# Kernel tuning notes

Hardware: AMD Instinct MI355X
Metric: run time of the kernel (lower is better)

The kernel has to match this reference:

```python
import jax, jax.numpy as jnp
import numpy as np

N, F, T, H, E, OUT, HEADS = 20000, 32, 12, 64, 320000, 12, 2


def setup_inputs() -> dict:
    key = jax.random.key(0)
    ks = iter(jax.random.split(key, 40))

    def nrm(shape, scale):
        return jax.random.normal(next(ks), shape, jnp.float32) * scale

    g0 = 2 * H + F   # gate input dim, cell 0
    g1 = 2 * H + H   # gate input dim, cell 1
    inp = {
        "x": nrm((N, F, T), 1.0),
        "edge_index": jax.random.randint(next(ks), (2, E), 0, N, dtype=jnp.int32),
        "edge_attr": jax.random.uniform(next(ks), (E, 2), dtype=jnp.float32),
        # cell 0: GCNConv + GRU gates (weights stored [in, out])
        "Wg0": nrm((F, H), F ** -0.5), "bg0": nrm((H,), 0.02),
        "Wu0": nrm((g0, H), g0 ** -0.5), "bu0": nrm((H,), 0.02),
        "Wr0": nrm((g0, H), g0 ** -0.5), "br0": nrm((H,), 0.02),
        "Wc0": nrm((g0, H), g0 ** -0.5), "bc0": nrm((H,), 0.02),
        # cell 1
        "Wg1": nrm((H, H), H ** -0.5), "bg1": nrm((H,), 0.02),
        "Wu1": nrm((g1, H), g1 ** -0.5), "bu1": nrm((H,), 0.02),
        "Wr1": nrm((g1, H), g1 ** -0.5), "br1": nrm((H,), 0.02),
        "Wc1": nrm((g1, H), g1 ** -0.5), "bc1": nrm((H,), 0.02),
        # temporal multi-head attention (torch layout: [out, in])
        "in_proj_w": nrm((3 * H, H), H ** -0.5), "in_proj_b": nrm((3 * H,), 0.02),
        "out_proj_w": nrm((H, H), H ** -0.5), "out_proj_b": nrm((H,), 0.02),
        # output head ([in, out])
        "out_w": nrm((H, OUT), H ** -0.5), "out_b": nrm((OUT,), 0.02),
    }
    return inp


def reference(x, edge_index, edge_attr,
              Wg0, bg0, Wu0, bu0, Wr0, br0, Wc0, bc0,
              Wg1, bg1, Wu1, bu1, Wr1, br1, Wc1, bc1,
              in_proj_w, in_proj_b, out_proj_w, out_proj_b,
              out_w, out_b):
    n, f, t = x.shape
    h_dim = Wg0.shape[1]
    src, dst = edge_index[0], edge_index[1]
    w = edge_attr[:, -1]

    # GCN normalization with self-loops (PyG gcn_norm)
    loop = jnp.arange(n)
    src_all = jnp.concatenate([src, loop])
    dst_all = jnp.concatenate([dst, loop])
    w_all = jnp.concatenate([w, jnp.ones((n,), x.dtype)])
    deg = jax.ops.segment_sum(w_all, dst_all, num_segments=n)
    dinv = jnp.where(deg > 0, jax.lax.rsqrt(deg), 0.0)
    norm = dinv[src_all] * w_all * dinv[dst_all]  # [E+N]

    def gcn(xi, W, b):
        xw = xi @ W  # [N, H]
        msg = norm[:, None] * xw[src_all]  # gather from sources
        return jax.ops.segment_sum(msg, dst_all, num_segments=n) + b

    def cell(xi, h, W, b, Wu, bu, Wr, br, Wc, bc):
        g = jax.nn.sigmoid(gcn(xi, W, b))
        zu = jnp.concatenate([xi, g, h], axis=-1)
        u = jax.nn.sigmoid(zu @ Wu + bu)
        r = jax.nn.sigmoid(zu @ Wr + br)
        zc = jnp.concatenate([xi, g, r * h], axis=-1)
        c = jnp.tanh(zc @ Wc + bc)
        return u * h + (1.0 - u) * c

    def step(carry, x_t):
        h0, h1 = carry
        h0 = cell(x_t, h0, Wg0, bg0, Wu0, bu0, Wr0, br0, Wc0, bc0)
        h1 = cell(h0, h1, Wg1, bg1, Wu1, bu1, Wr1, br1, Wc1, bc1)
        return (h0, h1), h1

    x_seq = jnp.transpose(x, (2, 0, 1))  # [T, N, F]
    h0 = jnp.zeros((n, h_dim), x.dtype)
    _, h_seq = jax.lax.scan(step, (h0, h0), x_seq)  # [T, N, H] (== [S, B, H])

    # temporal multi-head self-attention per node
    heads = HEADS
    dh = h_dim // heads
    qkv = h_seq @ in_proj_w.T + in_proj_b  # [T, N, 3H]
    q, k, v = jnp.split(qkv, 3, axis=-1)

    def split_heads(a):
        return jnp.transpose(a.reshape(t, n, heads, dh), (1, 2, 0, 3))  # [N, h, T, dh]

    q, k, v = split_heads(q), split_heads(k), split_heads(v)
    scores = jnp.einsum('nhtd,nhsd->nhts', q, k) / jnp.sqrt(jnp.asarray(dh, x.dtype))
    attn = jax.nn.softmax(scores, axis=-1)
    o = jnp.einsum('nhts,nhsd->nhtd', attn, v)
    o = jnp.transpose(o, (2, 0, 1, 3)).reshape(t, n, h_dim)
    o = o @ out_proj_w.T + out_proj_b  # [T, N, H]

    h_attn = o.mean(axis=0)  # agg='mean' over sequence -> [N, H]
    return h_attn @ out_w + out_b  # [N, OUT]
```

## Files before the change

kernel.cpp:

```cpp
#include <hip/hip_runtime.h>
#include <math.h>

#define NN 20000
#define FF 32
#define TT 12
#define HH 64
#define EE 320000
#define OUTD 12
#define CB1 1250

typedef __attribute__((ext_vector_type(8))) short short8;
typedef __attribute__((ext_vector_type(4))) float floatx4;

__device__ __forceinline__ float aexp2(float x) {
    float r; asm("v_exp_f32 %0, %1" : "=v"(r) : "v"(x)); return r;
}
__device__ __forceinline__ float arcp(float x) {
    float r; asm("v_rcp_f32 %0, %1" : "=v"(r) : "v"(x)); return r;
}
#define LOG2E 1.44269504088896f
__device__ __forceinline__ float fsig(float x) { return arcp(1.f + aexp2(-LOG2E * x)); }
__device__ __forceinline__ float ftanh(float x) {
    return fmaf(-2.f, arcp(1.f + aexp2(2.f * LOG2E * x)), 1.f);
}

__device__ __forceinline__ unsigned short bf16rne(float f) {
    union { float f; unsigned u; } v; v.f = f;
    unsigned u = v.u;
    u += 0x7fffu + ((u >> 16) & 1u);
    return (unsigned short)(u >> 16);
}
__device__ __forceinline__ float lof(unsigned v) {
    union { unsigned u; float f; } x; x.u = v << 16; return x.f;
}
__device__ __forceinline__ float hif(unsigned v) {
    union { unsigned u; float f; } x; x.u = v & 0xffff0000u; return x.f;
}
__device__ __forceinline__ unsigned packbf(float a, float b) {
    return (unsigned)bf16rne(a) | ((unsigned)bf16rne(b) << 16);
}

#define MFMA(a, b, c) __builtin_amdgcn_mfma_f32_16x16x32_bf16((a), (b), (c), 0, 0, 0)


__global__ void init_all(float* deg, int* cnt, float* h0f1, float* h1f1,
                         unsigned* h0s1u, unsigned* h1s0u) {
    int i = blockIdx.x * 256 + threadIdx.x;
    if (i < NN) { deg[i] = 1.0f; cnt[i] = 0; }
    if (i < NN * HH) { h0f1[i] = 0.f; h1f1[i] = 0.f; }
    if (i < NN * HH / 2) { h0s1u[i] = 0u; h1s0u[i] = 0u; }
}

__global__ void edge_accum_kernel(const int* ei, const float* ea, float* deg, int* cnt) {
    int e = blockIdx.x * 256 + threadIdx.x;
    if (e >= EE) return;
    int d = ei[EE + e];
    float w = ea[e * 2 + 1];
    atomicAdd(&deg[d], w);
    atomicAdd(&cnt[d], 1);
}

__global__ void scan_dinv(const int* cnt, int* rowptr, int* cursor,
                          const float* deg, float* dinv) {
    if (blockIdx.x != 0) {
        int i = (blockIdx.x - 1) * 1024 + threadIdx.x;
        if (i < NN) dinv[i] = rsqrtf(deg[i]);
        return;
    }
    __shared__ int wsum[16];
    int tid = threadIdx.x;
    int lane = tid & 63, w = tid >> 6;
    int run = 0;
    for (int base = 0; base < NN; base += 1024) {
        int idx = base + tid;
        int c = (idx < NN) ? cnt[idx] : 0;
        int v = c;
        #pragma unroll
        for (int off = 1; off < 64; off <<= 1) {
            int t = __shfl_up(v, off, 64);
            if (lane >= off) v += t;
        }
        if (lane == 63) wsum[w] = v;
        __syncthreads();
        if (tid < 16) {
            int x = wsum[tid];
            #pragma unroll
            for (int off = 1; off < 16; off <<= 1) {
                int t = __shfl_up(x, off, 64);
                if (tid >= off) x += t;
            }
            wsum[tid] = x;
        }
        __syncthreads();
        int waveoff = (w > 0) ? wsum[w - 1] : 0;
        int excl = run + waveoff + (v - c);
        if (idx < NN) { rowptr[idx] = excl; cursor[idx] = excl; }
        run += wsum[15];
        __syncthreads();
    }
    if (tid == 0) rowptr[NN] = run;
}

__global__ void fill_kernel(const int* ei, const float* ea, const float* dinv,
                            int* cursor, int2* colval) {
    int e = blockIdx.x * 256 + threadIdx.x;
    if (e >= EE) return;
    int s = ei[e], d = ei[EE + e];
    float w = ea[e * 2 + 1];
    int pos = atomicAdd(&cursor[d], 1);
    colval[pos] = make_int2(s, __float_as_int(dinv[s] * w * dinv[d]));
}

#define TPB 1250
#define WCB 336
__global__ void prep_misc(const float* __restrict__ x, unsigned short* __restrict__ xTs,
                          const float* Wg0, const float* Wu0, const float* Wr0, const float* Wc0,
                          const float* Wg1, const float* Wu1, const float* Wr1, const float* Wc1,
                          const float* ipw,
                          short* Wg0T, short* Wu0T, short* Wr0T, short* Wc0T,
                          short* Wg1T, short* Wu1T, short* Wr1T, short* Wc1T, short* ipwB,
                          const float* opw, const float* opb, const float* ow, const float* ob,
                          float* OW2, float* ob2) {
    int b = blockIdx.x;
    if (b < TPB) {
        __shared__ float tl[16 * 416];
        int n0 = b * 16;
        const float* xb = x + (size_t)n0 * 384;
        int tid = threadIdx.x;
        #pragma unroll
        for (int k = 0; k < 24; ++k) {
            int i = tid + 256 * k;
            float v = xb[i];
            int nn = i / 384;
            int rem = i - nn * 384;
            int f = rem / 12;
            int t2 = rem - f * 12;
            tl[nn * 416 + f * 13 + t2] = v;
        }
        __syncthreads();
        #pragma unroll
        for (int k = 0; k < 24; ++k) {
            int o = tid + 256 * k;
            int f = o & 31;
            int nn = (o >> 5) & 15;
            int t = o >> 9;
            xTs[(size_t)t * (NN * FF) + (size_t)(n0 + nn) * 32 + f] =
                bf16rne(tl[nn * 416 + f * 13 + t]);
        }
        return;
    }
    if (b < TPB + WCB) {
        int i = (b - TPB) * 256 + threadIdx.x;
        if (i < 2048) { int n = i / 32, k = i % 32; Wg0T[i] = (short)bf16rne(Wg0[k * 64 + n]); return; }
        i -= 2048;
        if (i < 10240) { int n = i / 160, k = i % 160; Wu0T[i] = (short)bf16rne(Wu0[k * 64 + n]); return; }
        i -= 10240;
        if (i < 10240) { int n = i / 160, k = i % 160; Wr0T[i] = (short)bf16rne(Wr0[k * 64 + n]); return; }
        i -= 10240;
        if (i < 10240) { int n = i / 160, k = i % 160; Wc0T[i] = (short)bf16rne(Wc0[k * 64 + n]); return; }
        i -= 10240;
        if (i < 4096) { int n = i / 64, k = i % 64; Wg1T[i] = (short)bf16rne(Wg1[k * 64 + n]); return; }
        i -= 4096;
        if (i < 12288) { int n = i / 192, k = i % 192; Wu1T[i] = (short)bf16rne(Wu1[k * 64 + n]); return; }
        i -= 12288;
        if (i < 12288) { int n = i / 192, k = i % 192; Wr1T[i] = (short)bf16rne(Wr1[k * 64 + n]); return; }
        i -= 12288;
        if (i < 12288) { int n = i / 192, k = i % 192; Wc1T[i] = (short)bf16rne(Wc1[k * 64 + n]); return; }
        i -= 12288;
        if (i < 12288) { ipwB[i] = (short)bf16rne(ipw[i]); }
        return;
    }
    {
        int i = (b - TPB - WCB) * 256 + threadIdx.x;
        if (i < 64 * OUTD) {
            int k = i / OUTD, d = i - k * OUTD;
            float acc = 0.f;
            for (int j = 0; j < 64; ++j) acc += opw[j * 64 + k] * ow[j * OUTD + d];
            OW2[i] = acc;
        } else if (i < 64 * OUTD + OUTD) {
            int d = i - 64 * OUTD;
            float acc = ob[d];
            for (int j = 0; j < 64; ++j) acc += opb[j] * ow[j * OUTD + d];
            ob2[d] = acc;
        }
    }
}

__global__ void gather_raw32(const unsigned short* __restrict__ xTs, const float* __restrict__ dinv,
                             const int* __restrict__ rowptr, const int2* __restrict__ colval,
                             unsigned short* __restrict__ aggxs) {
    const unsigned* src = (const unsigned*)(xTs + (size_t)blockIdx.y * NN * 32);
    unsigned* dst = (unsigned*)(aggxs + (size_t)blockIdx.y * NN * 32);
    int node = blockIdx.x * 16 + (threadIdx.x >> 4);
    int l2 = threadIdx.x & 15;
    float di = dinv[node];
    float dd = di * di;
    unsigned v = src[node * 16 + l2];
    float a0 = dd * lof(v), a1 = dd * hif(v);
    int s = rowptr[node], e = rowptr[node + 1];
    int j = s;
    for (; j + 3 < e; j += 4) {
        int2 cv0 = colval[j], cv1 = colval[j + 1], cv2 = colval[j + 2], cv3 = colval[j + 3];
        float w0 = __int_as_float(cv0.y), w1 = __int_as_float(cv1.y);
        float w2 = __int_as_float(cv2.y), w3 = __int_as_float(cv3.y);
        unsigned v0 = src[cv0.x * 16 + l2], v1 = src[cv1.x * 16 + l2];
        unsigned v2 = src[cv2.x * 16 + l2], v3 = src[cv3.x * 16 + l2];
        a0 += w0 * lof(v0) + w1 * lof(v1) + w2 * lof(v2) + w3 * lof(v3);
        a1 += w0 * hif(v0) + w1 * hif(v1) + w2 * hif(v2) + w3 * hif(v3);
    }
    for (; j < e; ++j) {
        int2 cv = colval[j];
        unsigned vv = src[cv.x * 16 + l2];
        float w = __int_as_float(cv.y);
        a0 += w * lof(vv); a1 += w * hif(vv);
    }
    dst[node * 16 + l2] = packbf(a0, a1);
}

__global__ void gather_g1(const unsigned short* __restrict__ y0s, const float* __restrict__ dinv,
                          const int* __restrict__ rowptr, const int2* __restrict__ colval,
                          const float* __restrict__ bg1, unsigned short* __restrict__ g1s) {
    const unsigned* yp = (const unsigned*)y0s;
    int node = blockIdx.x * 8 + (threadIdx.x >> 5);
    int l2 = threadIdx.x & 31;
    float di = dinv[node];
    float dd = di * di;
    unsigned v = yp[node * 32 + l2];
    float a0 = dd * lof(v), a1 = dd * hif(v);
    int s = rowptr[node], e = rowptr[node + 1];
    int j = s;
    for (; j + 3 < e; j += 4) {
        int2 cv0 = colval[j], cv1 = colval[j + 1], cv2 = colval[j + 2], cv3 = colval[j + 3];
        float w0 = __int_as_float(cv0.y), w1 = __int_as_float(cv1.y);
        float w2 = __int_as_float(cv2.y), w3 = __int_as_float(cv3.y);
        unsigned v0 = yp[cv0.x * 32 + l2], v1 = yp[cv1.x * 32 + l2];
        unsigned v2 = yp[cv2.x * 32 + l2], v3 = yp[cv3.x * 32 + l2];
        a0 += w0 * lof(v0) + w1 * lof(v1) + w2 * lof(v2) + w3 * lof(v3);
        a1 += w0 * hif(v0) + w1 * hif(v1) + w2 * hif(v2) + w3 * hif(v3);
    }
    for (; j < e; ++j) {
        int2 cv = colval[j];
        unsigned vv = yp[cv.x * 32 + l2];
        float w = __int_as_float(cv.y);
        a0 += w * lof(vv); a1 += w * hif(vv);
    }
    float g0v = fsig(a0 + bg1[2 * l2]);
    float g1v = fsig(a1 + bg1[2 * l2 + 1]);
    ((unsigned*)g1s)[node * 32 + l2] = packbf(g0v, g1v);
}


__launch_bounds__(256, 4)
__global__ void mfma_g0(const unsigned short* __restrict__ aggxs, const short* __restrict__ Wg0T,
                        const float* __restrict__ bg0, unsigned short* __restrict__ g0s) {
    int tid = threadIdx.x;
    int wv = tid >> 6, lane = tid & 63;
    int quad = lane >> 4, ln = lane & 15;
    int m0 = blockIdx.x * 64 + wv * 16;
    short8 af = *reinterpret_cast<const short8*>(aggxs + (size_t)(m0 + ln) * 32 + quad * 8);
    floatx4 z = {0.f, 0.f, 0.f, 0.f};
    floatx4 acc[4] = {z, z, z, z};
    #pragma unroll
    for (int ct = 0; ct < 4; ++ct) {
        short8 bf = *reinterpret_cast<const short8*>(Wg0T + (size_t)(ct * 16 + ln) * 32 + quad * 8);
        acc[ct] = MFMA(af, bf, acc[ct]);
    }
    #pragma unroll
    for (int ct = 0; ct < 4; ++ct) {
        int col = ct * 16 + ln;
        float bb = bg0[col];
        #pragma unroll
        for (int r = 0; r < 4; ++r) {
            int row = m0 + quad * 4 + r;
            g0s[(size_t)row * 64 + col] = bf16rne(fsig(acc[ct][r] + bb));
        }
    }
}


__device__ __forceinline__ void cell0_body(
    int m0, short* T,
    const unsigned short* __restrict__ xt, const unsigned short* __restrict__ g0,
    const float* __restrict__ h0f, const unsigned short* __restrict__ h0s,
    const short* __restrict__ Wu0T, const short* __restrict__ Wr0T,
    const short* __restrict__ Wc0T, const short* __restrict__ Wg1T,
    const float* __restrict__ bu0, const float* __restrict__ br0,
    const float* __restrict__ bc0,
    float* __restrict__ h0nf, unsigned short* __restrict__ h0ns,
    unsigned short* __restrict__ y0s) {
    int tid = threadIdx.x;
    int wv = tid >> 6, lane = tid & 63;
    int quad = lane >> 4, ln = lane & 15;
    int arow = m0 + ln;
    int col = wv * 16 + ln;

    short8 af[5];
    af[0] = *reinterpret_cast<const short8*>(xt + (size_t)arow * 32 + quad * 8);
    af[1] = *reinterpret_cast<const short8*>(g0 + (size_t)arow * 64 + quad * 8);
    af[2] = *reinterpret_cast<const short8*>(g0 + (size_t)arow * 64 + 32 + quad * 8);
    af[3] = *reinterpret_cast<const short8*>(h0s + (size_t)arow * 64 + quad * 8);
    af[4] = *reinterpret_cast<const short8*>(h0s + (size_t)arow * 64 + 32 + quad * 8);

    floatx4 z = {0.f, 0.f, 0.f, 0.f};
    floatx4 aU = z, aR = z;
    const short* bu = Wu0T + (size_t)col * 160;
    const short* br = Wr0T + (size_t)col * 160;
    #pragma unroll
    for (int kc = 0; kc < 5; ++kc) {
        int ko = kc * 32 + quad * 8;
        aU = MFMA(af[kc], *reinterpret_cast<const short8*>(bu + ko), aU);
        aR = MFMA(af[kc], *reinterpret_cast<const short8*>(br + ko), aR);
    }
    float bU = bu0[col], bR = br0[col];
    float uu[4], hv[4];
    #pragma unroll
    for (int r = 0; r < 4; ++r) {
        int grow = m0 + quad * 4 + r;
        uu[r] = fsig(aU[r] + bU);
        hv[r] = h0f[(size_t)grow * 64 + col];
        float rh = fsig(aR[r] + bR) * hv[r];
        T[(quad * 4 + r) * 72 + col] = (short)bf16rne(rh);
    }
    __syncthreads();

    short8 ar0 = *reinterpret_cast<const short8*>(T + ln * 72 + quad * 8);
    short8 ar1 = *reinterpret_cast<const short8*>(T + ln * 72 + 32 + quad * 8);
    floatx4 aC = z;
    const short* bc = Wc0T + (size_t)col * 160;
    #pragma unroll
    for (int kc = 0; kc < 3; ++kc)
        aC = MFMA(af[kc], *reinterpret_cast<const short8*>(bc + kc * 32 + quad * 8), aC);
    aC = MFMA(ar0, *reinterpret_cast<const short8*>(bc + 96 + quad * 8), aC);
    aC = MFMA(ar1, *reinterpret_cast<const short8*>(bc + 128 + quad * 8), aC);
    __syncthreads();

    float bC = bc0[col];
    #pragma unroll
    for (int r = 0; r < 4; ++r) {
        int grow = m0 + quad * 4 + r;
        float cv = ftanh(aC[r] + bC);
        float hn = uu[r] * hv[r] + (1.f - uu[r]) * cv;
        unsigned short hb = bf16rne(hn);
        h0nf[(size_t)grow * 64 + col] = hn;
        h0ns[(size_t)grow * 64 + col] = hb;
        T[(quad * 4 + r) * 72 + col] = (short)hb;
    }
    __syncthreads();

    short8 ah0 = *reinterpret_cast<const short8*>(T + ln * 72 + quad * 8);
    short8 ah1 = *reinterpret_cast<const short8*>(T + ln * 72 + 32 + quad * 8);
    floatx4 aY = z;
    const short* bg = Wg1T + (size_t)col * 64;
    aY = MFMA(ah0, *reinterpret_cast<const short8*>(bg + quad * 8), aY);
    aY = MFMA(ah1, *reinterpret_cast<const short8*>(bg + 32 + quad * 8), aY);
    #pragma unroll
    for (int r = 0; r < 4; ++r) {
        int grow = m0 + quad * 4 + r;
        y0s[(size_t)grow * 64 + col] = bf16rne(aY[r]);
    }
}

__device__ __forceinline__ void cell1_body(
    int m0, short* T,
    const unsigned short* __restrict__ h0s, const unsigned short* __restrict__ g1s,
    const float* __restrict__ h1f, const unsigned short* __restrict__ h1s,
    const short* __restrict__ Wu1T, const short* __restrict__ Wr1T,
    const short* __restrict__ Wc1T,
    const float* __restrict__ bu1, const float* __restrict__ br1,
    const float* __restrict__ bc1,
    float* __restrict__ h1nf, unsigned short* __restrict__ h1ns) {
    int tid = threadIdx.x;
    int wv = tid >> 6, lane = tid & 63;
    int quad = lane >> 4, ln = lane & 15;
    int arow = m0 + ln;
    int col = wv * 16 + ln;

    short8 af[6];
    af[0] = *reinterpret_cast<const short8*>(h0s + (size_t)arow * 64 + quad * 8);
    af[1] = *reinterpret_cast<const short8*>(h0s + (size_t)arow * 64 + 32 + quad * 8);
    af[2] = *reinterpret_cast<const short8*>(g1s + (size_t)arow * 64 + quad * 8);
    af[3] = *reinterpret_cast<const short8*>(g1s + (size_t)arow * 64 + 32 + quad * 8);
    af[4] = *reinterpret_cast<const short8*>(h1s + (size_t)arow * 64 + quad * 8);
    af[5] = *reinterpret_cast<const short8*>(h1s + (size_t)arow * 64 + 32 + quad * 8);

    floatx4 z = {0.f, 0.f, 0.f, 0.f};
    floatx4 aU = z, aR = z;
    const short* bu = Wu1T + (size_t)col * 192;
    const short* br = Wr1T + (size_t)col * 192;
    #pragma unroll
    for (int kc = 0; kc < 6; ++kc) {
        int ko = kc * 32 + quad * 8;
        aU = MFMA(af[kc], *reinterpret_cast<const short8*>(bu + ko), aU);
        aR = MFMA(af[kc], *reinterpret_cast<const short8*>(br + ko), aR);
    }
    float bU = bu1[col], bR = br1[col];
    float uu[4], hv[4];
    #pragma unroll
    for (int r = 0; r < 4; ++r) {
        int grow = m0 + quad * 4 + r;
        uu[r] = fsig(aU[r] + bU);
        hv[r] = h1f[(size_t)grow * 64 + col];
        float rh = fsig(aR[r] + bR) * hv[r];
        T[(quad * 4 + r) * 72 + col] = (short)bf16rne(rh);
    }
    __syncthreads();

    short8 ar0 = *reinterpret_cast<const short8*>(T + ln * 72 + quad * 8);
    short8 ar1 = *reinterpret_cast<const short8*>(T + ln * 72 + 32 + quad * 8);
    floatx4 aC = z;
    const short* bc = Wc1T + (size_t)col * 192;
    #pragma unroll
    for (int kc = 0; kc < 4; ++kc)
        aC = MFMA(af[kc], *reinterpret_cast<const short8*>(bc + kc * 32 + quad * 8), aC);
    aC = MFMA(ar0, *reinterpret_cast<const short8*>(bc + 128 + quad * 8), aC);
    aC = MFMA(ar1, *reinterpret_cast<const short8*>(bc + 160 + quad * 8), aC);

    float bC = bc1[col];
    #pragma unroll
    for (int r = 0; r < 4; ++r) {
        int grow = m0 + quad * 4 + r;
        float cv = ftanh(aC[r] + bC);
        float hn = uu[r] * hv[r] + (1.f - uu[r]) * cv;
        h1nf[(size_t)grow * 64 + col] = hn;
        h1ns[(size_t)grow * 64 + col] = bf16rne(hn);
    }
}

__launch_bounds__(256, 6)
__global__ void mfma_cell0(const unsigned short* xt, const unsigned short* g0,
                           const float* h0f, const unsigned short* h0s,
                           const short* Wu0T, const short* Wr0T, const short* Wc0T, const short* Wg1T,
                           const float* bu0, const float* br0, const float* bc0,
                           float* h0nf, unsigned short* h0ns, unsigned short* y0s) {
    __shared__ short T[16 * 72];
    cell0_body(blockIdx.x * 16, T,
               xt, g0, h0f, h0s, Wu0T, Wr0T, Wc0T, Wg1T, bu0, br0, bc0, h0nf, h0ns, y0s);
}

__launch_bounds__(256, 6)
__global__ void mfma_step(
    const unsigned short* h0s_cur, const unsigned short* g1s,
    const float* h1f_in, const unsigned short* h1s_in,
    const short* Wu1T, const short* Wr1T, const short* Wc1T,
    const float* bu1, const float* br1, const float* bc1,
    float* h1f_out, unsigned short* h1s_out,
    const unsigned short* xt_next, const unsigned short* g0_next, const float* h0f_cur,
    const short* Wu0T, const short* Wr0T, const short* Wc0T, const short* Wg1T,
    const float* bu0, const float* br0, const float* bc0,
    float* h0f_next, unsigned short* h0s_next, unsigned short* y0s) {
    __shared__ short T[16 * 72];
    if (blockIdx.x < CB1) {
        cell1_body(blockIdx.x * 16, T, h0s_cur, g1s, h1f_in, h1s_in,
                   Wu1T, Wr1T, Wc1T, bu1, br1, bc1, h1f_out, h1s_out);
    } else {
        cell0_body((blockIdx.x - CB1) * 16, T, xt_next, g0_next, h0f_cur, h0s_cur,
                   Wu0T, Wr0T, Wc0T, Wg1T, bu0, br0, bc0, h0f_next, h0s_next, y0s);
    }
}

__launch_bounds__(256, 5)
__global__ void attn_fused(const unsigned short* __restrict__ hseqs,
                           const short* __restrict__ ipwB, const float* __restrict__ ipb,
                           const float* __restrict__ OW2, const float* __restrict__ ob2,
                           float* __restrict__ out) {
    __shared__ unsigned short qtile[4][16 * 200];
    __shared__ float fbuf[4][64];
    __shared__ float wbuf[4][32];
    int wv = threadIdx.x >> 6, lane = threadIdx.x & 63;
    int node = blockIdx.x * 4 + wv;
    int quad = lane >> 4, ln = lane & 15;
    unsigned short* q = qtile[wv];
    float* sob = fbuf[wv];
    float* W = wbuf[wv];

    short8 zero8 = {0, 0, 0, 0, 0, 0, 0, 0};
    short8 af0 = zero8, af1 = zero8;
    if (ln < TT) {
        const unsigned short* hp = hseqs + ((size_t)ln * NN + node) * 64;
        af0 = *reinterpret_cast<const short8*>(hp + quad * 8);
        af1 = *reinterpret_cast<const short8*>(hp + 32 + quad * 8);
    }
    floatx4 z = {0.f, 0.f, 0.f, 0.f};
    #pragma unroll
    for (int ct = 0; ct < 12; ++ct) {
        const short* br = ipwB + (size_t)(ct * 16 + ln) * 64;
        floatx4 acc = MFMA(af0, *reinterpret_cast<const short8*>(br + quad * 8), z);
        acc = MFMA(af1, *reinterpret_cast<const short8*>(br + 32 + quad * 8), acc);
        int col = ct * 16 + ln;
        float bb = ipb[col];
        #pragma unroll
        for (int r = 0; r < 4; ++r)
            q[(quad * 4 + r) * 200 + col] = bf16rne(acc[r] + bb);
    }
    __threadfence_block();

    floatx4 sc[2];
    #pragma unroll
    for (int h = 0; h < 2; ++h) {
        short8 aQ = *reinterpret_cast<const short8*>(q + ln * 200 + h * 32 + quad * 8);
        short8 bK = *reinterpret_cast<const short8*>(q + ln * 200 + 64 + h * 32 + quad * 8);
        sc[h] = MFMA(aQ, bK, z);
    }
    const float scl = 0.17677669529663687f;
    bool colok = ln < 12;
    #pragma unroll
    for (int h = 0; h < 2; ++h) {
        float p[4];
        #pragma unroll
        for (int r = 0; r < 4; ++r) {
            float v = colok ? sc[h][r] * scl : -1e30f;
            float m = v;
            m = fmaxf(m, __shfl_xor(m, 1, 64));
            m = fmaxf(m, __shfl_xor(m, 2, 64));
            m = fmaxf(m, __shfl_xor(m, 4, 64));
            m = fmaxf(m, __shfl_xor(m, 8, 64));
            float e = colok ? aexp2(LOG2E * (v - m)) : 0.f;
            float s = e;
            s += __shfl_xor(s, 1, 64);
            s += __shfl_xor(s, 2, 64);
            s += __shfl_xor(s, 4, 64);
            s += __shfl_xor(s, 8, 64);
            p[r] = e * arcp(s);
        }
        float ts = (quad < 3) ? (p[0] + p[1] + p[2] + p[3]) : 0.f;
        ts += __shfl_xor(ts, 16, 64);
        ts += __shfl_xor(ts, 32, 64);
        if (quad == 0) W[h * 16 + ln] = ts * (1.f / 12.f);
    }
    __threadfence_block();

    {
        int d = lane, hd = d >> 5, dd = d & 31;
        float acc = 0.f;
        #pragma unroll
        for (int ts = 0; ts < 12; ++ts)
            acc += W[hd * 16 + ts] * lof((unsigned)q[ts * 200 + 128 + hd * 32 + dd]);
        sob[d] = acc;
    }
    __threadfence_block();

    if (lane < OUTD) {
        float acc = ob2[lane];
        #pragma unroll
        for (int k = 0; k < 64; ++k) acc += sob[k] * OW2[k * OUTD + lane];
        out[(size_t)node * OUTD + lane] = acc;
    }
}


extern "C" void kernel_launch(void* const* d_in, const int* in_sizes, int n_in,
                              void* d_out, int out_size, void* d_ws, size_t ws_size,
                              hipStream_t stream) {
    const float* x   = (const float*)d_in[0];
    const int*   ei  = (const int*)d_in[1];
    const float* ea  = (const float*)d_in[2];
    const float* Wg0 = (const float*)d_in[3];
    const float* bg0 = (const float*)d_in[4];
    const float* Wu0 = (const float*)d_in[5];
    const float* bu0 = (const float*)d_in[6];
    const float* Wr0 = (const float*)d_in[7];
    const float* br0 = (const float*)d_in[8];
    const float* Wc0 = (const float*)d_in[9];
    const float* bc0 = (const float*)d_in[10];
    const float* Wg1 = (const float*)d_in[11];
    const float* bg1 = (const float*)d_in[12];
    const float* Wu1 = (const float*)d_in[13];
    const float* bu1 = (const float*)d_in[14];
    const float* Wr1 = (const float*)d_in[15];
    const float* br1 = (const float*)d_in[16];
    const float* Wc1 = (const float*)d_in[17];
    const float* bc1 = (const float*)d_in[18];
    const float* ipw = (const float*)d_in[19];
    const float* ipb = (const float*)d_in[20];
    const float* opw = (const float*)d_in[21];
    const float* opb = (const float*)d_in[22];
    const float* ow  = (const float*)d_in[23];
    const float* ob  = (const float*)d_in[24];
    float* out = (float*)d_out;

    char* p = (char*)d_ws;
    auto alloc = [&](size_t bytes) { char* r = p; p += (bytes + 255) & ~(size_t)255; return (void*)r; };
    unsigned short* hseqs = (unsigned short*)alloc((size_t)TT * NN * HH * 2);
    unsigned short* h1s0  = (unsigned short*)alloc((size_t)NN * HH * 2);
    short* Wg0T = (short*)alloc((size_t)64 * 32 * 2);
    short* Wu0T = (short*)alloc((size_t)64 * 160 * 2);
    short* Wr0T = (short*)alloc((size_t)64 * 160 * 2);
    short* Wc0T = (short*)alloc((size_t)64 * 160 * 2);
    short* Wg1T = (short*)alloc((size_t)64 * 64 * 2);
    short* Wu1T = (short*)alloc((size_t)64 * 192 * 2);
    short* Wr1T = (short*)alloc((size_t)64 * 192 * 2);
    short* Wc1T = (short*)alloc((size_t)64 * 192 * 2);
    short* ipwB = (short*)alloc((size_t)192 * 64 * 2);
    float* OW2  = (float*)alloc((size_t)64 * OUTD * 4);
    float* ob2  = (float*)alloc((size_t)OUTD * 4);
    float* dinv   = (float*)alloc((size_t)NN * 4);
    int*   rowptr = (int*)  alloc((size_t)(NN + 1) * 4);
    int2*  colval = (int2*) alloc((size_t)EE * 8);
    unsigned short* xTs   = (unsigned short*)alloc((size_t)TT * NN * FF * 2);
    unsigned short* aggxs = (unsigned short*)alloc((size_t)TT * NN * FF * 2);
    unsigned short* g0s   = (unsigned short*)alloc((size_t)TT * NN * HH * 2);
    float* deg    = (float*)alloc((size_t)NN * 4);
    int*   cnt    = (int*)  alloc((size_t)NN * 4);
    int*   cursor = (int*)  alloc((size_t)NN * 4);
    unsigned short* y0s = (unsigned short*)alloc((size_t)NN * HH * 2);
    unsigned short* g1s = (unsigned short*)alloc((size_t)NN * HH * 2);
    float* h0f0 = (float*)alloc((size_t)NN * HH * 4);
    float* h0f1 = (float*)alloc((size_t)NN * HH * 4);
    float* h1f0 = (float*)alloc((size_t)NN * HH * 4);
    float* h1f1 = (float*)alloc((size_t)NN * HH * 4);
    unsigned short* h0s0 = (unsigned short*)alloc((size_t)NN * HH * 2);
    unsigned short* h0s1 = (unsigned short*)alloc((size_t)NN * HH * 2);
    (void)ws_size;

    init_all<<<(NN * HH + 255) / 256, 256, 0, stream>>>(
        deg, cnt, h0f1, h1f1, (unsigned*)h0s1, (unsigned*)h1s0);
    edge_accum_kernel<<<(EE + 255) / 256, 256, 0, stream>>>(ei, ea, deg, cnt);
    scan_dinv<<<1 + (NN + 1023) / 1024, 1024, 0, stream>>>(cnt, rowptr, cursor, deg, dinv);
    fill_kernel<<<(EE + 255) / 256, 256, 0, stream>>>(ei, ea, dinv, cursor, colval);
    prep_misc<<<TPB + WCB + 4, 256, 0, stream>>>(
        x, xTs,
        Wg0, Wu0, Wr0, Wc0, Wg1, Wu1, Wr1, Wc1, ipw,
        Wg0T, Wu0T, Wr0T, Wc0T, Wg1T, Wu1T, Wr1T, Wc1T, ipwB,
        opw, opb, ow, ob, OW2, ob2);

    gather_raw32<<<dim3(NN / 16, TT), 256, 0, stream>>>(xTs, dinv, rowptr, colval, aggxs);
    mfma_g0<<<(TT * NN) / 64, 256, 0, stream>>>(aggxs, Wg0T, bg0, g0s);

    float* h0f[2] = {h0f0, h0f1};
    unsigned short* h0s[2] = {h0s0, h0s1};
    float* h1f[2] = {h1f0, h1f1};

    mfma_cell0<<<CB1, 256, 0, stream>>>(
        xTs, g0s, h0f[1], h0s[1], Wu0T, Wr0T, Wc0T, Wg1T, bu0, br0, bc0,
        h0f[0], h0s[0], y0s);

    for (int t = 0; t < TT; ++t) {
        gather_g1<<<NN / 8, 256, 0, stream>>>(y0s, dinv, rowptr, colval, bg1, g1s);
        int tn = (t < TT - 1) ? (t + 1) : t;
        int grid = (t < TT - 1) ? 2 * CB1 : CB1;
        mfma_step<<<grid, 256, 0, stream>>>(
            h0s[t & 1], g1s, h1f[(t + 1) & 1],
            (t == 0) ? h1s0 : (hseqs + (size_t)(t - 1) * NN * HH),
            Wu1T, Wr1T, Wc1T, bu1, br1, bc1,
            h1f[t & 1], hseqs + (size_t)t * NN * HH,
            xTs + (size_t)tn * NN * FF, g0s + (size_t)tn * NN * HH, h0f[t & 1],
            Wu0T, Wr0T, Wc0T, Wg1T, bu0, br0, bc0,
            h0f[(t + 1) & 1], h0s[(t + 1) & 1], y0s);
    }

    attn_fused<<<NN / 4, 256, 0, stream>>>(hseqs, ipwB, ipb, OW2, ob2, out);
}
```

Before: 807.3 us.

## Software-pipeline recurrent cells and graph gather into one launch per stage

```diff
diff --git a/kernel.cpp b/kernel.cpp
--- a/kernel.cpp
+++ b/kernel.cpp
@@ -8,6 +8,7 @@
 #define EE 320000
 #define OUTD 12
 #define CB1 1250
+#define GB  2500
 
 typedef __attribute__((ext_vector_type(8))) short short8;
 typedef __attribute__((ext_vector_type(4))) float floatx4;
@@ -44,11 +45,11 @@
 
 
 __global__ void init_all(float* deg, int* cnt, float* h0f1, float* h1f1,
-                         unsigned* h0s1u, unsigned* h1s0u) {
+                         unsigned* h0s2u, unsigned* h1s0u) {
     int i = blockIdx.x * 256 + threadIdx.x;
     if (i < NN) { deg[i] = 1.0f; cnt[i] = 0; }
     if (i < NN * HH) { h0f1[i] = 0.f; h1f1[i] = 0.f; }
-    if (i < NN * HH / 2) { h0s1u[i] = 0u; h1s0u[i] = 0u; }
+    if (i < NN * HH / 2) { h0s2u[i] = 0u; h1s0u[i] = 0u; }
 }
 
 __global__ void edge_accum_kernel(const int* ei, const float* ea, float* deg, int* cnt) {
@@ -217,11 +218,12 @@
     dst[node * 16 + l2] = packbf(a0, a1);
 }
 
-__global__ void gather_g1(const unsigned short* __restrict__ y0s, const float* __restrict__ dinv,
-                          const int* __restrict__ rowptr, const int2* __restrict__ colval,
-                          const float* __restrict__ bg1, unsigned short* __restrict__ g1s) {
+__device__ __forceinline__ void gather_g1_body(
+    int blk, const unsigned short* __restrict__ y0s, const float* __restrict__ dinv,
+    const int* __restrict__ rowptr, const int2* __restrict__ colval,
+    const float* __restrict__ bg1, unsigned short* __restrict__ g1s) {
     const unsigned* yp = (const unsigned*)y0s;
-    int node = blockIdx.x * 8 + (threadIdx.x >> 5);
+    int node = blk * 8 + (threadIdx.x >> 5);
     int l2 = threadIdx.x & 31;
     float di = dinv[node];
     float dd = di * di;
@@ -426,36 +428,44 @@
     }
 }
 
+
+struct PipeArgs {
+    const float* dinv; const int* rowptr; const int2* colval;
+    const short* Wu0T; const short* Wr0T; const short* Wc0T; const short* Wg1T;
+    const float* bu0; const float* br0; const float* bc0;
+    const short* Wu1T; const short* Wr1T; const short* Wc1T;
+    const float* bu1; const float* br1; const float* bc1; const float* bg1;
+    int c0n;
+    const unsigned short* c0_xt; const unsigned short* c0_g0;
+    const float* c0_hf_in; const unsigned short* c0_hs_in;
+    float* c0_hf_out; unsigned short* c0_hs_out; unsigned short* c0_y0_out;
+    int gn;
+    const unsigned short* g_y0; unsigned short* g_g1;
+    int c1n;
+    const unsigned short* c1_h0s; const unsigned short* c1_g1;
+    const float* c1_hf_in; const unsigned short* c1_hs_in;
+    float* c1_hf_out; unsigned short* c1_hs_out;
+};
+
 __launch_bounds__(256, 6)
-__global__ void mfma_cell0(const unsigned short* xt, const unsigned short* g0,
-                           const float* h0f, const unsigned short* h0s,
-                           const short* Wu0T, const short* Wr0T, const short* Wc0T, const short* Wg1T,
-                           const float* bu0, const float* br0, const float* bc0,
-                           float* h0nf, unsigned short* h0ns, unsigned short* y0s) {
+__global__ void pipe_step(PipeArgs A) {
     __shared__ short T[16 * 72];
-    cell0_body(blockIdx.x * 16, T,
-               xt, g0, h0f, h0s, Wu0T, Wr0T, Wc0T, Wg1T, bu0, br0, bc0, h0nf, h0ns, y0s);
-}
-
-__launch_bounds__(256, 6)
-__global__ void mfma_step(
-    const unsigned short* h0s_cur, const unsigned short* g1s,
-    const float* h1f_in, const unsigned short* h1s_in,
-    const short* Wu1T, const short* Wr1T, const short* Wc1T,
-    const float* bu1, const float* br1, const float* bc1,
-    float* h1f_out, unsigned short* h1s_out,
-    const unsigned short* xt_next, const unsigned short* g0_next, const float* h0f_cur,
-    const short* Wu0T, const short* Wr0T, const short* Wc0T, const short* Wg1T,
-    const float* bu0, const float* br0, const float* bc0,
-    float* h0f_next, unsigned short* h0s_next, unsigned short* y0s) {
-    __shared__ short T[16 * 72];
-    if (blockIdx.x < CB1) {
-        cell1_body(blockIdx.x * 16, T, h0s_cur, g1s, h1f_in, h1s_in,
-                   Wu1T, Wr1T, Wc1T, bu1, br1, bc1, h1f_out, h1s_out);
-    } else {
-        cell0_body((blockIdx.x - CB1) * 16, T, xt_next, g0_next, h0f_cur, h0s_cur,
-                   Wu0T, Wr0T, Wc0T, Wg1T, bu0, br0, bc0, h0f_next, h0s_next, y0s);
-    }
+    int b = blockIdx.x;
+    if (b < A.c0n) {
+        cell0_body(b * 16, T, A.c0_xt, A.c0_g0, A.c0_hf_in, A.c0_hs_in,
+                   A.Wu0T, A.Wr0T, A.Wc0T, A.Wg1T, A.bu0, A.br0, A.bc0,
+                   A.c0_hf_out, A.c0_hs_out, A.c0_y0_out);
+        return;
+    }
+    b -= A.c0n;
+    if (b < A.gn) {
+        gather_g1_body(b, A.g_y0, A.dinv, A.rowptr, A.colval, A.bg1, A.g_g1);
+        return;
+    }
+    b -= A.gn;
+    cell1_body(b * 16, T, A.c1_h0s, A.c1_g1, A.c1_hf_in, A.c1_hs_in,
+               A.Wu1T, A.Wr1T, A.Wc1T, A.bu1, A.br1, A.bc1,
+               A.c1_hf_out, A.c1_hs_out);
 }
 
 __launch_bounds__(256, 5)
@@ -602,18 +612,21 @@
     float* deg    = (float*)alloc((size_t)NN * 4);
     int*   cnt    = (int*)  alloc((size_t)NN * 4);
     int*   cursor = (int*)  alloc((size_t)NN * 4);
-    unsigned short* y0s = (unsigned short*)alloc((size_t)NN * HH * 2);
-    unsigned short* g1s = (unsigned short*)alloc((size_t)NN * HH * 2);
+    unsigned short* y0sA = (unsigned short*)alloc((size_t)NN * HH * 2);
+    unsigned short* y0sB = (unsigned short*)alloc((size_t)NN * HH * 2);
+    unsigned short* g1sA = (unsigned short*)alloc((size_t)NN * HH * 2);
+    unsigned short* g1sB = (unsigned short*)alloc((size_t)NN * HH * 2);
     float* h0f0 = (float*)alloc((size_t)NN * HH * 4);
     float* h0f1 = (float*)alloc((size_t)NN * HH * 4);
     float* h1f0 = (float*)alloc((size_t)NN * HH * 4);
     float* h1f1 = (float*)alloc((size_t)NN * HH * 4);
     unsigned short* h0s0 = (unsigned short*)alloc((size_t)NN * HH * 2);
     unsigned short* h0s1 = (unsigned short*)alloc((size_t)NN * HH * 2);
+    unsigned short* h0s2 = (unsigned short*)alloc((size_t)NN * HH * 2);
     (void)ws_size;
 
     init_all<<<(NN * HH + 255) / 256, 256, 0, stream>>>(
-        deg, cnt, h0f1, h1f1, (unsigned*)h0s1, (unsigned*)h1s0);
+        deg, cnt, h0f1, h1f1, (unsigned*)h0s2, (unsigned*)h1s0);
     edge_accum_kernel<<<(EE + 255) / 256, 256, 0, stream>>>(ei, ea, deg, cnt);
     scan_dinv<<<1 + (NN + 1023) / 1024, 1024, 0, stream>>>(cnt, rowptr, cursor, deg, dinv);
     fill_kernel<<<(EE + 255) / 256, 256, 0, stream>>>(ei, ea, dinv, cursor, colval);
@@ -626,26 +639,56 @@
     gather_raw32<<<dim3(NN / 16, TT), 256, 0, stream>>>(xTs, dinv, rowptr, colval, aggxs);
     mfma_g0<<<(TT * NN) / 64, 256, 0, stream>>>(aggxs, Wg0T, bg0, g0s);
 
-    float* h0f[2] = {h0f0, h0f1};
-    unsigned short* h0s[2] = {h0s0, h0s1};
-    float* h1f[2] = {h1f0, h1f1};
-
-    mfma_cell0<<<CB1, 256, 0, stream>>>(
-        xTs, g0s, h0f[1], h0s[1], Wu0T, Wr0T, Wc0T, Wg1T, bu0, br0, bc0,
-        h0f[0], h0s[0], y0s);
-
-    for (int t = 0; t < TT; ++t) {
-        gather_g1<<<NN / 8, 256, 0, stream>>>(y0s, dinv, rowptr, colval, bg1, g1s);
-        int tn = (t < TT - 1) ? (t + 1) : t;
-        int grid = (t < TT - 1) ? 2 * CB1 : CB1;
-        mfma_step<<<grid, 256, 0, stream>>>(
-            h0s[t & 1], g1s, h1f[(t + 1) & 1],
-            (t == 0) ? h1s0 : (hseqs + (size_t)(t - 1) * NN * HH),
-            Wu1T, Wr1T, Wc1T, bu1, br1, bc1,
-            h1f[t & 1], hseqs + (size_t)t * NN * HH,
-            xTs + (size_t)tn * NN * FF, g0s + (size_t)tn * NN * HH, h0f[t & 1],
-            Wu0T, Wr0T, Wc0T, Wg1T, bu0, br0, bc0,
-            h0f[(t + 1) & 1], h0s[(t + 1) & 1], y0s);
+    float* h0fB[2] = {h0f0, h0f1};
+    unsigned short* h0sB[3] = {h0s0, h0s1, h0s2};
+    float* h1fB[2] = {h1f0, h1f1};
+    unsigned short* y0B[2] = {y0sA, y0sB};
+    unsigned short* g1B[2] = {g1sA, g1sB};
+
+    PipeArgs base;
+    base.dinv = dinv; base.rowptr = rowptr; base.colval = colval;
+    base.Wu0T = Wu0T; base.Wr0T = Wr0T; base.Wc0T = Wc0T; base.Wg1T = Wg1T;
+    base.bu0 = bu0; base.br0 = br0; base.bc0 = bc0;
+    base.Wu1T = Wu1T; base.Wr1T = Wr1T; base.Wc1T = Wc1T;
+    base.bu1 = bu1; base.br1 = br1; base.bc1 = bc1; base.bg1 = bg1;
+
+    for (int l = 0; l <= TT + 1; ++l) {
+        PipeArgs A = base;
+        int tc0 = l, tg = l - 1, tc1 = l - 2;
+
+        A.c0n = (tc0 < TT) ? CB1 : 0;
+        if (A.c0n) {
+            A.c0_xt = xTs + (size_t)tc0 * NN * FF;
+            A.c0_g0 = g0s + (size_t)tc0 * NN * HH;
+            A.c0_hf_in = h0fB[(tc0 + 1) & 1];
+            A.c0_hs_in = h0sB[(tc0 + 2) % 3];
+            A.c0_hf_out = h0fB[tc0 & 1];
+            A.c0_hs_out = h0sB[tc0 % 3];
+            A.c0_y0_out = y0B[tc0 & 1];
+        } else {
+            A.c0_xt = xTs; A.c0_g0 = g0s; A.c0_hf_in = h0fB[0]; A.c0_hs_in = h0sB[0];
+            A.c0_hf_out = h0fB[0]; A.c0_hs_out = h0sB[0]; A.c0_y0_out = y0B[0];
+        }
+
+        A.gn = (tg >= 0 && tg < TT) ? GB : 0;
+        if (A.gn) { A.g_y0 = y0B[tg & 1]; A.g_g1 = g1B[tg & 1]; }
+        else { A.g_y0 = y0B[0]; A.g_g1 = g1B[0]; }
+
+        A.c1n = (tc1 >= 0 && tc1 < TT) ? CB1 : 0;
+        if (A.c1n) {
+            A.c1_h0s = h0sB[tc1 % 3];
+            A.c1_g1 = g1B[tc1 & 1];
+            A.c1_hf_in = h1fB[(tc1 + 1) & 1];
+            A.c1_hs_in = (tc1 == 0) ? h1s0 : (hseqs + (size_t)(tc1 - 1) * NN * HH);
+            A.c1_hf_out = h1fB[tc1 & 1];
+            A.c1_hs_out = hseqs + (size_t)tc1 * NN * HH;
+        } else {
+            A.c1_h0s = h0sB[0]; A.c1_g1 = g1B[0]; A.c1_hf_in = h1fB[0];
+            A.c1_hs_in = h1s0; A.c1_hf_out = h1fB[0]; A.c1_hs_out = hseqs;
+        }
+
+        int grid = A.c0n + A.gn + A.c1n;
+        pipe_step<<<grid, 256, 0, stream>>>(A);
     }
 
     attn_fused<<<NN / 4, 256, 0, stream>>>(hseqs, ipwB, ipb, OW2, ob2, out);
```

Result: no change. 799.6 us (-1.0%).
